# Kernel optimization log

Hardware: AMD Instinct MI355X
Metric: run time of the kernel (lower is better)

## Reference

```python
import jax, jax.numpy as jnp
import numpy as np

M, F_IN, F_OUT, K = 8192, 32, 32, 5


def setup_inputs() -> dict:
    key = jax.random.key(0)
    k1, k2, k3 = jax.random.split(key, 3)
    x = jax.random.normal(k1, (M, F_IN), dtype=jnp.float32)
    # scale so spectral radius ~O(1); real simplicial Laplacians have bounded spectrum
    L = jax.random.normal(k2, (M, M), dtype=jnp.float32) / jnp.sqrt(jnp.float32(M))
    # xavier-uniform-like scale for W (gain for relu)
    gain = jnp.sqrt(jnp.float32(2.0))
    bound = gain * jnp.sqrt(jnp.float32(6.0 / (F_IN + F_OUT)))
    W = jax.random.uniform(k3, (K, F_IN, F_OUT), dtype=jnp.float32,
                           minval=-bound, maxval=bound)
    return {"x": x, "L": L, "W": W}


def reference(x, L, W):
    """y = sum_{k=0}^{K-1} L^k @ x @ W[k].

    Math identical to the torch module, but computed via the recursive
    propagation z_k = L @ z_{k-1} (z_0 = x), i.e. O(K*M^2*F) instead of
    forming dense matrix powers L^k (O(K*M^3)).
    """
    y0 = x @ W[0]                      # [M, F_out], k = 0 term (L^0 = I)

    def body(z, Wk):
        z = L @ z                      # z_k = L @ z_{k-1}, [M, F_in]
        return z, z @ Wk               # term_k = L^k x W[k], [M, F_out]

    _, terms = jax.lax.scan(body, x, W[1:])   # terms: [K-1, M, F_out]
    return y0 + terms.sum(axis=0)
```

## Files before the change

kernel.cpp:

```cpp
#include <hip/hip_runtime.h>

typedef unsigned short u16;
typedef unsigned int u32;
typedef __bf16 bf16x8 __attribute__((ext_vector_type(8)));
typedef float f32x4 __attribute__((ext_vector_type(4)));
typedef u32 u32x2 __attribute__((ext_vector_type(2)));
typedef u32 u32x4 __attribute__((ext_vector_type(4)));

#define M_DIM 8192
#define S_SPLIT 8
#define CHUNK 1024
#define CROWS 16
#define PBM 64

__device__ __forceinline__ u16 f2bf(float f) {
  u32 u = __builtin_bit_cast(u32, f);
  u += 0x7FFFu + ((u >> 16) & 1u);
  return (u16)(u >> 16);
}

union Frag {
  bf16x8 f;
  u16 s[8];
  u32x2 h2[2];
  u32x4 q;
};


__global__ __launch_bounds__(256) void head_kernel(
    const float* __restrict__ x, const float* __restrict__ W0,
    float* __restrict__ y_out, u16* __restrict__ zbt0) {
  __shared__ float Ws[1024];
  __shared__ u16 zsb[256][34];
  const int t = threadIdx.x;
  for (int i = t; i < 1024; i += 256) Ws[i] = W0[i];
  const int m = blockIdx.x * 256 + t;
  float z[32];
  const float4* xr = (const float4*)(x + (size_t)m * 32);
#pragma unroll
  for (int i = 0; i < 8; i++) {
    float4 v = xr[i];
    z[4 * i] = v.x; z[4 * i + 1] = v.y; z[4 * i + 2] = v.z; z[4 * i + 3] = v.w;
  }
#pragma unroll
  for (int c = 0; c < 32; c++) zsb[t][c] = f2bf(z[c]);
  __syncthreads();
  float acc[32];
#pragma unroll
  for (int j = 0; j < 32; j++) acc[j] = 0.f;
#pragma unroll
  for (int c = 0; c < 32; c++) {
#pragma unroll
    for (int j = 0; j < 32; j++) acc[j] += z[c] * Ws[c * 32 + j];
  }
  float4* yo = (float4*)(y_out + (size_t)m * 32);
#pragma unroll
  for (int i = 0; i < 8; i++) {
    float4 v; v.x = acc[4 * i]; v.y = acc[4 * i + 1];
    v.z = acc[4 * i + 2]; v.w = acc[4 * i + 3];
    yo[i] = v;
  }
  const int lane = t & 63, w = t >> 6;
  const int l15 = lane & 15, l4 = lane >> 4;
#pragma unroll
  for (int i = 0; i < 4; i++) {
    int tile = w * 4 + i;
    int ktl = tile >> 1, nt = tile & 1;
    Frag fr;
#pragma unroll
    for (int j = 0; j < 8; j++) fr.s[j] = zsb[ktl * 32 + 8 * l4 + j][nt * 16 + l15];
    size_t kt_g = (size_t)blockIdx.x * 8 + ktl;
    *(u32x4*)(zbt0 + ((kt_g * 2 + nt) * 64 + lane) * 8) = fr.q;
  }
}

__global__ __launch_bounds__(256) void conv_kernel(
    const float* __restrict__ L, const u16* __restrict__ zbt0,
    u16* __restrict__ Lbt, float* __restrict__ z_part) {
  __shared__ u16 At[CROWS][1032];
  __shared__ float red[4][16][33];
  const int t = threadIdx.x;
  const int lane = t & 63, w = t >> 6;
  const int l15 = lane & 15, l4 = lane >> 4;
  const int bx = blockIdx.x;
  const int by = blockIdx.y;
  const int r0 = bx * CROWS;
  const size_t kbase = (size_t)by * CHUNK;

#pragma unroll
  for (int rr = 0; rr < 4; rr++) {
    const int row = w * 4 + rr;
    const float* src = L + (size_t)(r0 + row) * M_DIM + kbase + lane * 4;
#pragma unroll
    for (int seg = 0; seg < 4; seg++) {
      float4 v = *(const float4*)(src + seg * 256);
      u32x2 p;
      p[0] = (u32)f2bf(v.x) | ((u32)f2bf(v.y) << 16);
      p[1] = (u32)f2bf(v.z) | ((u32)f2bf(v.w) << 16);
      *(u32x2*)&At[row][seg * 256 + lane * 4] = p;
    }
  }
  __syncthreads();

  f32x4 acc0 = {0.f, 0.f, 0.f, 0.f};
  f32x4 acc1 = {0.f, 0.f, 0.f, 0.f};
#pragma unroll
  for (int i = 0; i < 8; i++) {
    const int ktl = w * 8 + i;
    Frag fa;
    fa.q = *(const u32x4*)&At[l15][ktl * 32 + 8 * l4];
    *(u32x4*)(Lbt + ((size_t)(bx * 256 + by * 32 + ktl)) * 512 + lane * 8) = fa.q;
    Frag fb0, fb1;
    size_t bo = ((size_t)((by * 32 + ktl) * 2)) * 512 + lane * 8;
    fb0.q = *(const u32x4*)(zbt0 + bo);
    fb1.q = *(const u32x4*)(zbt0 + bo + 512);
    acc0 = __builtin_amdgcn_mfma_f32_16x16x32_bf16(fa.f, fb0.f, acc0, 0, 0, 0);
    acc1 = __builtin_amdgcn_mfma_f32_16x16x32_bf16(fa.f, fb1.f, acc1, 0, 0, 0);
  }
#pragma unroll
  for (int r = 0; r < 4; r++) {
    red[w][4 * l4 + r][l15] = acc0[r];
    red[w][4 * l4 + r][l15 + 16] = acc1[r];
  }
  __syncthreads();
  const int orow = t >> 4, ocol = t & 15;
  float v0 = red[0][orow][ocol] + red[1][orow][ocol] +
             red[2][orow][ocol] + red[3][orow][ocol];
  float v1 = red[0][orow][ocol + 16] + red[1][orow][ocol + 16] +
             red[2][orow][ocol + 16] + red[3][orow][ocol + 16];
  float* zp = z_part + (size_t)by * (M_DIM * 32) + (size_t)(r0 + orow) * 32;
  zp[ocol] = v0;
  zp[ocol + 16] = v1;
}

__global__ __launch_bounds__(256) void passk_kernel(
    const u16* __restrict__ Lbt, const u16* __restrict__ zbt,
    float* __restrict__ z_part) {
  const int t = threadIdx.x;
  const int lane = t & 63, w = t >> 6;
  const int l15 = lane & 15, l4 = lane >> 4;
  const int bx = blockIdx.x;
  const int by = blockIdx.y;
  const int rt = bx * 4 + w;

  const u16* ap = Lbt + ((size_t)rt * 256 + by * 32) * 512 + lane * 8;
  const u16* bp = zbt + ((size_t)(by * 32) * 2) * 512 + lane * 8;

  f32x4 acc0 = {0.f, 0.f, 0.f, 0.f};
  f32x4 acc1 = {0.f, 0.f, 0.f, 0.f};
#pragma unroll 8
  for (int kt = 0; kt < 32; kt++) {
    Frag fa, fb0, fb1;
    fa.q = *(const u32x4*)(ap + (size_t)kt * 512);
    fb0.q = *(const u32x4*)(bp + (size_t)kt * 1024);
    fb1.q = *(const u32x4*)(bp + (size_t)kt * 1024 + 512);
    acc0 = __builtin_amdgcn_mfma_f32_16x16x32_bf16(fa.f, fb0.f, acc0, 0, 0, 0);
    acc1 = __builtin_amdgcn_mfma_f32_16x16x32_bf16(fa.f, fb1.f, acc1, 0, 0, 0);
  }
  float* zp = z_part + (size_t)by * (M_DIM * 32) +
              (size_t)(bx * PBM + w * 16 + 4 * l4) * 32 + l15;
#pragma unroll
  for (int r = 0; r < 4; r++) {
    zp[r * 32] = acc0[r];
    zp[r * 32 + 16] = acc1[r];
  }
}

template <bool LAST>
__global__ __launch_bounds__(256) void reduce_kernel(
    const float* __restrict__ zp, const float* __restrict__ Wk,
    const float* __restrict__ y_in, float* __restrict__ y_out,
    u16* __restrict__ zbt_out) {
  __shared__ float Ws[1024];
  __shared__ float zs[64][33];
  __shared__ u16 zsb[64][34];
  const int t = threadIdx.x;
  for (int i = t; i < 1024; i += 256) Ws[i] = Wk[i];
  const int ml = t >> 2, cg = t & 3;
  const int m = blockIdx.x * 64 + ml;
  const float* p = zp + (size_t)m * 32 + cg * 8;
  float z8[8];
  {
    float4 lo = *(const float4*)p;
    float4 hi = *(const float4*)(p + 4);
    z8[0] = lo.x; z8[1] = lo.y; z8[2] = lo.z; z8[3] = lo.w;
    z8[4] = hi.x; z8[5] = hi.y; z8[6] = hi.z; z8[7] = hi.w;
  }
#pragma unroll
  for (int s = 1; s < S_SPLIT; s++) {
    const float* ps = p + (size_t)s * (M_DIM * 32);
    float4 lo = *(const float4*)ps;
    float4 hi = *(const float4*)(ps + 4);
    z8[0] += lo.x; z8[1] += lo.y; z8[2] += lo.z; z8[3] += lo.w;
    z8[4] += hi.x; z8[5] += hi.y; z8[6] += hi.z; z8[7] += hi.w;
  }
#pragma unroll
  for (int i = 0; i < 8; i++) {
    zs[ml][cg * 8 + i] = z8[i];
    zsb[ml][cg * 8 + i] = f2bf(z8[i]);
  }
  __syncthreads();
  float acc[8];
  {
    const float4* yi = (const float4*)(y_in + (size_t)m * 32 + cg * 8);
    float4 a0 = yi[0], a1 = yi[1];
    acc[0] = a0.x; acc[1] = a0.y; acc[2] = a0.z; acc[3] = a0.w;
    acc[4] = a1.x; acc[5] = a1.y; acc[6] = a1.z; acc[7] = a1.w;
  }
#pragma unroll
  for (int c = 0; c < 32; c++) {
    float zv = zs[ml][c];
    const float* wr = Ws + c * 32 + cg * 8;
#pragma unroll
    for (int j = 0; j < 8; j++) acc[j] += zv * wr[j];
  }
  float4* yo = (float4*)(y_out + (size_t)m * 32 + cg * 8);
  float4 o0, o1;
  o0.x = acc[0]; o0.y = acc[1]; o0.z = acc[2]; o0.w = acc[3];
  o1.x = acc[4]; o1.y = acc[5]; o1.z = acc[6]; o1.w = acc[7];
  yo[0] = o0; yo[1] = o1;

  if (!LAST) {
    const int lane = t & 63, w = t >> 6;
    const int l15 = lane & 15, l4 = lane >> 4;
    const int ktl = w >> 1, nt = w & 1;
    Frag fr;
#pragma unroll
    for (int j = 0; j < 8; j++)
      fr.s[j] = zsb[ktl * 32 + 8 * l4 + j][nt * 16 + l15];
    size_t kt_g = (size_t)blockIdx.x * 2 + ktl;
    *(u32x4*)(zbt_out + ((kt_g * 2 + nt) * 64 + lane) * 8) = fr.q;
  }
}

extern "C" void kernel_launch(void* const* d_in, const int* in_sizes, int n_in,
                              void* d_out, int out_size, void* d_ws,
                              size_t ws_size, hipStream_t stream) {
  const float* x = (const float*)d_in[0];
  const float* L = (const float*)d_in[1];
  const float* W = (const float*)d_in[2];
  float* y = (float*)d_out;
  char* ws = (char*)d_ws;

  const size_t ZT = (size_t)512 << 10;
  u16* zbt0 = (u16*)(ws + 0 * ZT);
  u16* zbt1 = (u16*)(ws + 1 * ZT);
  u16* zbt2 = (u16*)(ws + 2 * ZT);
  u16* zbt3 = (u16*)(ws + 3 * ZT);
  float* z_part = (float*)(ws + ((size_t)2 << 20));
  float* y_acc = (float*)(ws + ((size_t)10 << 20));
  u16* Lbt = (u16*)(ws + ((size_t)12 << 20));

  head_kernel<<<32, 256, 0, stream>>>(x, W, y_acc, zbt0);
  conv_kernel<<<dim3(512, S_SPLIT), 256, 0, stream>>>(L, zbt0, Lbt, z_part);
  reduce_kernel<false><<<128, 256, 0, stream>>>(z_part, W + 1024, y_acc, y_acc, zbt1);
  passk_kernel<<<dim3(128, S_SPLIT), 256, 0, stream>>>(Lbt, zbt1, z_part);
  reduce_kernel<false><<<128, 256, 0, stream>>>(z_part, W + 2048, y_acc, y_acc, zbt2);
  passk_kernel<<<dim3(128, S_SPLIT), 256, 0, stream>>>(Lbt, zbt2, z_part);
  reduce_kernel<false><<<128, 256, 0, stream>>>(z_part, W + 3072, y_acc, y_acc, zbt3);
  passk_kernel<<<dim3(128, S_SPLIT), 256, 0, stream>>>(Lbt, zbt3, z_part);
  reduce_kernel<true><<<128, 256, 0, stream>>>(z_part, W + 4096, y_acc, y, (u16*)0);
}
```

Measured before the change: 199.8 us.

## Fuse split-K propagation passes with reduction and W projection into one kernel

Replaces each passk+reduce kernel pair for steps 2-4 with a single fpass kernel. In it, eight waves split K across the full row range, their partials are summed in shared memory, and the same block applies W[k], updates y and emits the bf16 swizzled z for the next step. This removes the fp32 z_part round trip through global memory and half the launches. Each block now covers only 16 rows with 512 threads, and the small per-block epilogue does a serial 32-term dot per thread. The change also uses the builtin bf16 conversion and nontemporal loads for L in the conversion kernel.

```diff
diff --git a/kernel.cpp b/kernel.cpp
--- a/kernel.cpp
+++ b/kernel.cpp
@@ -11,12 +11,9 @@
 #define S_SPLIT 8
 #define CHUNK 1024
 #define CROWS 16
-#define PBM 64
 
 __device__ __forceinline__ u16 f2bf(float f) {
-  u32 u = __builtin_bit_cast(u32, f);
-  u += 0x7FFFu + ((u >> 16) & 1u);
-  return (u16)(u >> 16);
+  return __builtin_bit_cast(u16, (__bf16)f);
 }
 
 union Frag {
@@ -93,10 +90,10 @@
     const float* src = L + (size_t)(r0 + row) * M_DIM + kbase + lane * 4;
 #pragma unroll
     for (int seg = 0; seg < 4; seg++) {
-      float4 v = *(const float4*)(src + seg * 256);
+      f32x4 v = __builtin_nontemporal_load((const f32x4*)(src + seg * 256));
       u32x2 p;
-      p[0] = (u32)f2bf(v.x) | ((u32)f2bf(v.y) << 16);
-      p[1] = (u32)f2bf(v.z) | ((u32)f2bf(v.w) << 16);
+      p[0] = (u32)f2bf(v[0]) | ((u32)f2bf(v[1]) << 16);
+      p[1] = (u32)f2bf(v[2]) | ((u32)f2bf(v[3]) << 16);
       *(u32x2*)&At[row][seg * 256 + lane * 4] = p;
     }
   }
@@ -133,18 +130,87 @@
   zp[ocol + 16] = v1;
 }
 
-__global__ __launch_bounds__(256) void passk_kernel(
+__global__ __launch_bounds__(256) void reduce_kernel(
+    const float* __restrict__ zp, const float* __restrict__ Wk,
+    const float* __restrict__ y_in, float* __restrict__ y_out,
+    u16* __restrict__ zbt_out) {
+  __shared__ float Ws[1024];
+  __shared__ float zs[64][33];
+  __shared__ u16 zsb[64][34];
+  const int t = threadIdx.x;
+  for (int i = t; i < 1024; i += 256) Ws[i] = Wk[i];
+  const int ml = t >> 2, cg = t & 3;
+  const int m = blockIdx.x * 64 + ml;
+  const float* p = zp + (size_t)m * 32 + cg * 8;
+  float z8[8];
+  {
+    float4 lo = *(const float4*)p;
+    float4 hi = *(const float4*)(p + 4);
+    z8[0] = lo.x; z8[1] = lo.y; z8[2] = lo.z; z8[3] = lo.w;
+    z8[4] = hi.x; z8[5] = hi.y; z8[6] = hi.z; z8[7] = hi.w;
+  }
+#pragma unroll
+  for (int s = 1; s < S_SPLIT; s++) {
+    const float* ps = p + (size_t)s * (M_DIM * 32);
+    float4 lo = *(const float4*)ps;
+    float4 hi = *(const float4*)(ps + 4);
+    z8[0] += lo.x; z8[1] += lo.y; z8[2] += lo.z; z8[3] += lo.w;
+    z8[4] += hi.x; z8[5] += hi.y; z8[6] += hi.z; z8[7] += hi.w;
+  }
+#pragma unroll
+  for (int i = 0; i < 8; i++) {
+    zs[ml][cg * 8 + i] = z8[i];
+    zsb[ml][cg * 8 + i] = f2bf(z8[i]);
+  }
+  __syncthreads();
+  float acc[8];
+  {
+    const float4* yi = (const float4*)(y_in + (size_t)m * 32 + cg * 8);
+    float4 a0 = yi[0], a1 = yi[1];
+    acc[0] = a0.x; acc[1] = a0.y; acc[2] = a0.z; acc[3] = a0.w;
+    acc[4] = a1.x; acc[5] = a1.y; acc[6] = a1.z; acc[7] = a1.w;
+  }
+#pragma unroll
+  for (int c = 0; c < 32; c++) {
+    float zv = zs[ml][c];
+    const float* wr = Ws + c * 32 + cg * 8;
+#pragma unroll
+    for (int j = 0; j < 8; j++) acc[j] += zv * wr[j];
+  }
+  float4* yo = (float4*)(y_out + (size_t)m * 32 + cg * 8);
+  float4 o0, o1;
+  o0.x = acc[0]; o0.y = acc[1]; o0.z = acc[2]; o0.w = acc[3];
+  o1.x = acc[4]; o1.y = acc[5]; o1.z = acc[6]; o1.w = acc[7];
+  yo[0] = o0; yo[1] = o1;
+
+  const int lane = t & 63, w = t >> 6;
+  const int l15 = lane & 15, l4 = lane >> 4;
+  const int ktl = w >> 1, nt = w & 1;
+  Frag fr;
+#pragma unroll
+  for (int j = 0; j < 8; j++)
+    fr.s[j] = zsb[ktl * 32 + 8 * l4 + j][nt * 16 + l15];
+  size_t kt_g = (size_t)blockIdx.x * 2 + ktl;
+  *(u32x4*)(zbt_out + ((kt_g * 2 + nt) * 64 + lane) * 8) = fr.q;
+}
+
+template <bool LAST>
+__global__ __launch_bounds__(512, 4) void fpass_kernel(
     const u16* __restrict__ Lbt, const u16* __restrict__ zbt,
-    float* __restrict__ z_part) {
+    const float* __restrict__ Wk, const float* __restrict__ y_in,
+    float* __restrict__ y_out, u16* __restrict__ zbt_out) {
+  __shared__ float red[8][16][33];
+  __shared__ float Ws[1024];
+  __shared__ float zs[16][33];
+  __shared__ u16 zsb[16][36];
   const int t = threadIdx.x;
   const int lane = t & 63, w = t >> 6;
   const int l15 = lane & 15, l4 = lane >> 4;
   const int bx = blockIdx.x;
-  const int by = blockIdx.y;
-  const int rt = bx * 4 + w;
-
-  const u16* ap = Lbt + ((size_t)rt * 256 + by * 32) * 512 + lane * 8;
-  const u16* bp = zbt + ((size_t)(by * 32) * 2) * 512 + lane * 8;
+  for (int i = t; i < 1024; i += 512) Ws[i] = Wk[i];
+
+  const u16* ap = Lbt + ((size_t)bx * 256 + w * 32) * 512 + lane * 8;
+  const u16* bp = zbt + (size_t)(w * 32) * 1024 + lane * 8;
 
   f32x4 acc0 = {0.f, 0.f, 0.f, 0.f};
   f32x4 acc1 = {0.f, 0.f, 0.f, 0.f};
@@ -157,79 +223,32 @@
     acc0 = __builtin_amdgcn_mfma_f32_16x16x32_bf16(fa.f, fb0.f, acc0, 0, 0, 0);
     acc1 = __builtin_amdgcn_mfma_f32_16x16x32_bf16(fa.f, fb1.f, acc1, 0, 0, 0);
   }
-  float* zp = z_part + (size_t)by * (M_DIM * 32) +
-              (size_t)(bx * PBM + w * 16 + 4 * l4) * 32 + l15;
 #pragma unroll
   for (int r = 0; r < 4; r++) {
-    zp[r * 32] = acc0[r];
-    zp[r * 32 + 16] = acc1[r];
-  }
-}
-
-template <bool LAST>
-__global__ __launch_bounds__(256) void reduce_kernel(
-    const float* __restrict__ zp, const float* __restrict__ Wk,
-    const float* __restrict__ y_in, float* __restrict__ y_out,
-    u16* __restrict__ zbt_out) {
-  __shared__ float Ws[1024];
-  __shared__ float zs[64][33];
-  __shared__ u16 zsb[64][34];
-  const int t = threadIdx.x;
-  for (int i = t; i < 1024; i += 256) Ws[i] = Wk[i];
-  const int ml = t >> 2, cg = t & 3;
-  const int m = blockIdx.x * 64 + ml;
-  const float* p = zp + (size_t)m * 32 + cg * 8;
-  float z8[8];
-  {
-    float4 lo = *(const float4*)p;
-    float4 hi = *(const float4*)(p + 4);
-    z8[0] = lo.x; z8[1] = lo.y; z8[2] = lo.z; z8[3] = lo.w;
-    z8[4] = hi.x; z8[5] = hi.y; z8[6] = hi.z; z8[7] = hi.w;
-  }
-#pragma unroll
-  for (int s = 1; s < S_SPLIT; s++) {
-    const float* ps = p + (size_t)s * (M_DIM * 32);
-    float4 lo = *(const float4*)ps;
-    float4 hi = *(const float4*)(ps + 4);
-    z8[0] += lo.x; z8[1] += lo.y; z8[2] += lo.z; z8[3] += lo.w;
-    z8[4] += hi.x; z8[5] += hi.y; z8[6] += hi.z; z8[7] += hi.w;
-  }
-#pragma unroll
-  for (int i = 0; i < 8; i++) {
-    zs[ml][cg * 8 + i] = z8[i];
-    zsb[ml][cg * 8 + i] = f2bf(z8[i]);
-  }
-  __syncthreads();
-  float acc[8];
-  {
-    const float4* yi = (const float4*)(y_in + (size_t)m * 32 + cg * 8);
-    float4 a0 = yi[0], a1 = yi[1];
-    acc[0] = a0.x; acc[1] = a0.y; acc[2] = a0.z; acc[3] = a0.w;
-    acc[4] = a1.x; acc[5] = a1.y; acc[6] = a1.z; acc[7] = a1.w;
-  }
-#pragma unroll
-  for (int c = 0; c < 32; c++) {
-    float zv = zs[ml][c];
-    const float* wr = Ws + c * 32 + cg * 8;
-#pragma unroll
-    for (int j = 0; j < 8; j++) acc[j] += zv * wr[j];
-  }
-  float4* yo = (float4*)(y_out + (size_t)m * 32 + cg * 8);
-  float4 o0, o1;
-  o0.x = acc[0]; o0.y = acc[1]; o0.z = acc[2]; o0.w = acc[3];
-  o1.x = acc[4]; o1.y = acc[5]; o1.z = acc[6]; o1.w = acc[7];
-  yo[0] = o0; yo[1] = o1;
-
-  if (!LAST) {
-    const int lane = t & 63, w = t >> 6;
-    const int l15 = lane & 15, l4 = lane >> 4;
-    const int ktl = w >> 1, nt = w & 1;
+    red[w][4 * l4 + r][l15] = acc0[r];
+    red[w][4 * l4 + r][l15 + 16] = acc1[r];
+  }
+  __syncthreads();
+  const int row = t >> 5, j = t & 31;
+  float v = 0.f;
+#pragma unroll
+  for (int s = 0; s < 8; s++) v += red[s][row][j];
+  zs[row][j] = v;
+  zsb[row][j] = f2bf(v);
+  __syncthreads();
+  float yv = y_in[(size_t)(bx * 16 + row) * 32 + j];
+#pragma unroll
+  for (int c = 0; c < 32; c++) yv += zs[row][c] * Ws[c * 32 + j];
+  y_out[(size_t)(bx * 16 + row) * 32 + j] = yv;
+
+  if (!LAST && t < 64) {
+    const int nt = t >> 5, li = t & 31;
+    const int kt = bx >> 1, h = bx & 1;
     Frag fr;
 #pragma unroll
-    for (int j = 0; j < 8; j++)
-      fr.s[j] = zsb[ktl * 32 + 8 * l4 + j][nt * 16 + l15];
-    size_t kt_g = (size_t)blockIdx.x * 2 + ktl;
-    *(u32x4*)(zbt_out + ((kt_g * 2 + nt) * 64 + lane) * 8) = fr.q;
+    for (int jj = 0; jj < 8; jj++)
+      fr.s[jj] = zsb[8 * (li >> 4) + jj][nt * 16 + (li & 15)];
+    *(u32x4*)(zbt_out + (size_t)((kt * 2 + nt) * 64 + 32 * h + li) * 8) = fr.q;
   }
 }
 
@@ -253,11 +272,8 @@
 
   head_kernel<<<32, 256, 0, stream>>>(x, W, y_acc, zbt0);
   conv_kernel<<<dim3(512, S_SPLIT), 256, 0, stream>>>(L, zbt0, Lbt, z_part);
-  reduce_kernel<false><<<128, 256, 0, stream>>>(z_part, W + 1024, y_acc, y_acc, zbt1);
-  passk_kernel<<<dim3(128, S_SPLIT), 256, 0, stream>>>(Lbt, zbt1, z_part);
-  reduce_kernel<false><<<128, 256, 0, stream>>>(z_part, W + 2048, y_acc, y_acc, zbt2);
-  passk_kernel<<<dim3(128, S_SPLIT), 256, 0, stream>>>(Lbt, zbt2, z_part);
-  reduce_kernel<false><<<128, 256, 0, stream>>>(z_part, W + 3072, y_acc, y_acc, zbt3);
-  passk_kernel<<<dim3(128, S_SPLIT), 256, 0, stream>>>(Lbt, zbt3, z_part);
-  reduce_kernel<true><<<128, 256, 0, stream>>>(z_part, W + 4096, y_acc, y, (u16*)0);
-}
+  reduce_kernel<<<128, 256, 0, stream>>>(z_part, W + 1024, y_acc, y_acc, zbt1);
+  fpass_kernel<false><<<512, 512, 0, stream>>>(Lbt, zbt1, W + 2048, y_acc, y_acc, zbt2);
+  fpass_kernel<false><<<512, 512, 0, stream>>>(Lbt, zbt2, W + 3072, y_acc, y_acc, zbt3);
+  fpass_kernel<true><<<512, 512, 0, stream>>>(Lbt, zbt3, W + 4096, y_acc, y, (u16*)0);
+}
```

Result: faster. 186.5 us (-6.7%).
